# Performance work log

Measured on AMD Instinct MI355X. Metric: run time of the kernel, lower is better.

Reference implementation:

```python
import jax, jax.numpy as jnp
import numpy as np

B, U, SIZE, D_ATT = 8, 1024, 1024, 1024
NEG_INF = -1e38


def setup_inputs() -> dict:
    key = jax.random.key(0)
    ks = jax.random.split(key, 16)
    s = 0.02
    return {
        "x": jax.random.normal(ks[0], (B, U, SIZE), jnp.float32),
        "time_decay": jax.random.normal(ks[1], (D_ATT,), jnp.float32),
        "time_first": jax.random.normal(ks[2], (D_ATT,), jnp.float32),
        "time_mix_key": jax.random.uniform(ks[3], (1, 1, SIZE), jnp.float32),
        "time_mix_value": jax.random.uniform(ks[4], (1, 1, SIZE), jnp.float32),
        "time_mix_receptance": jax.random.uniform(ks[5], (1, 1, SIZE), jnp.float32),
        "W_key": jax.random.normal(ks[6], (SIZE, D_ATT), jnp.float32) * s,
        "b_key": jax.random.normal(ks[7], (D_ATT,), jnp.float32) * s,
        "W_value": jax.random.normal(ks[8], (SIZE, D_ATT), jnp.float32) * s,
        "b_value": jax.random.normal(ks[9], (D_ATT,), jnp.float32) * s,
        "W_receptance": jax.random.normal(ks[10], (SIZE, D_ATT), jnp.float32) * s,
        "b_receptance": jax.random.normal(ks[11], (D_ATT,), jnp.float32) * s,
        "W_output": jax.random.normal(ks[12], (D_ATT, SIZE), jnp.float32) * s,
        "b_output": jax.random.normal(ks[13], (SIZE,), jnp.float32) * s,
    }


def wkv_scan(time_decay, time_first, k, v):
    """Numerically-stable RWKV WKV recurrence. k, v: (B, U, D)."""
    w = -jnp.exp(time_decay)  # (D,)

    def step(carry, kv):
        a, b, p = carry  # each (B, D): numerator, denominator, running max
        kt, vt = kv      # (B, D)
        # output at step t (includes time_first bonus for current token)
        q = jnp.maximum(p, time_first + kt)
        e1 = jnp.exp(p - q)
        e2 = jnp.exp(time_first + kt - q)
        out = (e1 * a + e2 * vt) / (e1 * b + e2)
        # state update (decay by w)
        q2 = jnp.maximum(p + w, kt)
        e1 = jnp.exp(p + w - q2)
        e2 = jnp.exp(kt - q2)
        return (e1 * a + e2 * vt, e1 * b + e2, q2), out

    Bb, Uu, Dd = k.shape
    init = (
        jnp.zeros((Bb, Dd), k.dtype),
        jnp.zeros((Bb, Dd), k.dtype),
        jnp.full((Bb, Dd), NEG_INF, k.dtype),
    )
    _, out = jax.lax.scan(step, init, (k.transpose(1, 0, 2), v.transpose(1, 0, 2)))
    return out.transpose(1, 0, 2)  # (B, U, D)


def reference(x, time_decay, time_first, time_mix_key, time_mix_value,
              time_mix_receptance, W_key, b_key, W_value, b_value,
              W_receptance, b_receptance, W_output, b_output):
    # time_shift: shifted[t] = x[t-1], shifted[0] = 0
    shifted = jnp.pad(x, ((0, 0), (1, 0), (0, 0)))[:, :-1, :]
    k_in = x * time_mix_key + shifted * (1.0 - time_mix_key)
    v_in = x * time_mix_value + shifted * (1.0 - time_mix_value)
    r_in = x * time_mix_receptance + shifted * (1.0 - time_mix_receptance)
    k = jnp.einsum("bus,sd->bud", k_in, W_key) + b_key
    v = jnp.einsum("bus,sd->bud", v_in, W_value) + b_value
    r = jax.nn.sigmoid(jnp.einsum("bus,sd->bud", r_in, W_receptance) + b_receptance)
    wkv = wkv_scan(time_decay, time_first, k, v)
    out = jnp.einsum("bud,ds->bus", r * wkv, W_output) + b_output
    return out
```

## Files before the change

kernel.cpp:

```cpp
#include <hip/hip_runtime.h>
#include <cstdint>
#include <cstddef>

#define B_DIM 8
#define U_DIM 1024
#define SD    1024
#define M_DIM (B_DIM * U_DIM)
#define NC 32
#define CT 32

typedef __attribute__((ext_vector_type(8))) short short8;
typedef __attribute__((ext_vector_type(4))) float f32x4;

typedef __attribute__((address_space(3))) void       lds_t;
typedef const __attribute__((address_space(1))) void glb_t;

__device__ __forceinline__ ushort f2bf(float f) {
    union { float f; uint32_t u; } c; c.f = f;
    uint32_t r = (c.u + 0x7FFFu + ((c.u >> 16) & 1u)) >> 16;
    return (ushort)r;
}
__device__ __forceinline__ float bf2f(ushort h) {
    union { float f; uint32_t u; } c; c.u = ((uint32_t)h) << 16; return c.f;
}

__global__ __launch_bounds__(256)
void wtrans_kernel(const float* __restrict__ Wk, const float* __restrict__ Wv,
                   const float* __restrict__ Wr, const float* __restrict__ Wo,
                   ushort* __restrict__ WT)
{
    __shared__ float t[32][33];
    const float* W = (blockIdx.z == 0) ? Wk : (blockIdx.z == 1) ? Wv
                   : (blockIdx.z == 2) ? Wr : Wo;
    ushort* o = WT + (size_t)blockIdx.z * SD * SD;
    const int tx = threadIdx.x & 31, ty = threadIdx.x >> 5;
    const int k0 = blockIdx.y * 32, n0 = blockIdx.x * 32;
    #pragma unroll
    for (int i = 0; i < 4; ++i)
        t[ty + i * 8][tx] = W[(size_t)(k0 + ty + i * 8) * SD + n0 + tx];
    __syncthreads();
    #pragma unroll
    for (int i = 0; i < 4; ++i)
        o[(size_t)(n0 + ty + i * 8) * SD + k0 + tx] = f2bf(t[tx][ty + i * 8]);
}

__global__ __launch_bounds__(256)
void mix3_kernel(const float* __restrict__ x,
                 const float* __restrict__ mk, const float* __restrict__ mv,
                 const float* __restrict__ mr,
                 ushort* __restrict__ Ak, ushort* __restrict__ Av,
                 ushort* __restrict__ Ar)
{
    const int idx = blockIdx.x * 256 + threadIdx.x;
    const int m = idx >> 8;
    const int s = (idx & 255) << 2;
    const float4 xv = *(const float4*)&x[(size_t)m * SD + s];
    float4 sh = make_float4(0.f, 0.f, 0.f, 0.f);
    if (m & (U_DIM - 1)) sh = *(const float4*)&x[(size_t)(m - 1) * SD + s];
    const float4 dx = make_float4(xv.x - sh.x, xv.y - sh.y, xv.z - sh.z, xv.w - sh.w);
    const size_t off = (size_t)m * SD + s;

    float4 mx;
    ushort4 o;
    mx = *(const float4*)&mk[s];
    o.x = f2bf(sh.x + mx.x * dx.x); o.y = f2bf(sh.y + mx.y * dx.y);
    o.z = f2bf(sh.z + mx.z * dx.z); o.w = f2bf(sh.w + mx.w * dx.w);
    *(ushort4*)&Ak[off] = o;
    mx = *(const float4*)&mv[s];
    o.x = f2bf(sh.x + mx.x * dx.x); o.y = f2bf(sh.y + mx.y * dx.y);
    o.z = f2bf(sh.z + mx.z * dx.z); o.w = f2bf(sh.w + mx.w * dx.w);
    *(ushort4*)&Av[off] = o;
    mx = *(const float4*)&mr[s];
    o.x = f2bf(sh.x + mx.x * dx.x); o.y = f2bf(sh.y + mx.y * dx.y);
    o.z = f2bf(sh.z + mx.z * dx.z); o.w = f2bf(sh.w + mx.w * dx.w);
    *(ushort4*)&Ar[off] = o;
}

__global__ __launch_bounds__(256)
void mix_kernel(const float* __restrict__ x, const float* __restrict__ mix,
                ushort* __restrict__ outA)
{
    const int idx = blockIdx.x * 256 + threadIdx.x;
    const int m = idx >> 8;
    const int s = (idx & 255) << 2;
    const float4 xv = *(const float4*)&x[(size_t)m * SD + s];
    float4 sh = make_float4(0.f, 0.f, 0.f, 0.f);
    if (m & (U_DIM - 1)) sh = *(const float4*)&x[(size_t)(m - 1) * SD + s];
    const float4 mx = *(const float4*)&mix[s];
    ushort4 o;
    o.x = f2bf(sh.x + mx.x * (xv.x - sh.x));
    o.y = f2bf(sh.y + mx.y * (xv.y - sh.y));
    o.z = f2bf(sh.z + mx.z * (xv.z - sh.z));
    o.w = f2bf(sh.w + mx.w * (xv.w - sh.w));
    *(ushort4*)&outA[(size_t)m * SD + s] = o;
}

template<int FUSED>
__global__ __launch_bounds__(256)
void gemm_bf16(const ushort* __restrict__ Abase, const ushort* __restrict__ WT,
               const float* __restrict__ b0, const float* __restrict__ b1,
               const float* __restrict__ b2, void* __restrict__ Cbase)
{
    __shared__ ushort As[2][4096];
    __shared__ ushort Bs[2][4096];

    const int tid = threadIdx.x;
    const int wv = tid >> 6, ln = tid & 63;
    const int m0 = blockIdx.x * 128, n0 = blockIdx.y * 128;
    const int wm = (wv >> 1) * 64, wn = (wv & 1) * 64;

    const ushort* A; const ushort* BT; const float* bias; void* Cout; int dosig;
    if (FUSED == 3) {
        const int z = blockIdx.z;
        A    = Abase + (size_t)z * ((size_t)M_DIM * SD);
        BT   = WT + (size_t)z * ((size_t)SD * SD);
        bias = (z == 0) ? b0 : (z == 1) ? b1 : b2;
        Cout = (void*)((ushort*)Cbase + (size_t)z * ((size_t)M_DIM * SD));
        dosig = (z == 2);
    } else {
        A = Abase; BT = WT; bias = b0; Cout = Cbase; dosig = (FUSED == 1);
    }

    const int srow = tid >> 2;
    const int sq   = tid & 3;
    const int sqs  = sq ^ ((srow >> 1) & 3);
    const size_t gA = (size_t)(m0 + srow) * SD + sqs * 8;
    const size_t gB = (size_t)(n0 + srow) * SD + sqs * 8;
    char* const asb = (char*)As + wv * 1024;
    char* const bsb = (char*)Bs + wv * 1024;

    const int lr  = ln & 15;
    const int lq  = ln >> 4;
    const int sqr = (lr >> 1) & 3;
    const int kof = (lq ^ sqr) * 8;

    f32x4 acc[4][4];
    #pragma unroll
    for (int i = 0; i < 4; ++i)
        #pragma unroll
        for (int j = 0; j < 4; ++j)
            acc[i][j] = (f32x4){0.f, 0.f, 0.f, 0.f};

#define STAGE(buf, k0)                                                              \
    do {                                                                            \
        __builtin_amdgcn_global_load_lds((glb_t*)(A + gA + (k0)),                   \
            (lds_t*)(asb + (buf) * 8192), 16, 0, 0);                                \
        __builtin_amdgcn_global_load_lds((glb_t*)(A + gA + (size_t)64 * SD + (k0)), \
            (lds_t*)(asb + (buf) * 8192 + 4096), 16, 0, 0);                         \
        __builtin_amdgcn_global_load_lds((glb_t*)(BT + gB + (k0)),                  \
            (lds_t*)(bsb + (buf) * 8192), 16, 0, 0);                                \
        __builtin_amdgcn_global_load_lds((glb_t*)(BT + gB + (size_t)64 * SD + (k0)),\
            (lds_t*)(bsb + (buf) * 8192 + 4096), 16, 0, 0);                         \
    } while (0)

#define COMPUTE(buf)                                                                \
    do {                                                                            \
        short8 af[4], bfr[4];                                                       \
        _Pragma("unroll")                                                           \
        for (int mt = 0; mt < 4; ++mt)                                              \
            af[mt] = *(const short8*)&As[buf][(wm + mt * 16 + lr) * 32 + kof];      \
        _Pragma("unroll")                                                           \
        for (int nt = 0; nt < 4; ++nt)                                              \
            bfr[nt] = *(const short8*)&Bs[buf][(wn + nt * 16 + lr) * 32 + kof];     \
        _Pragma("unroll")                                                           \
        for (int mt = 0; mt < 4; ++mt)                                              \
            _Pragma("unroll")                                                       \
            for (int nt = 0; nt < 4; ++nt)                                          \
                acc[mt][nt] = __builtin_amdgcn_mfma_f32_16x16x32_bf16(              \
                    af[mt], bfr[nt], acc[mt][nt], 0, 0, 0);                         \
    } while (0)

    STAGE(0, 0);
    __syncthreads();
    for (int t = 0; t < 30; t += 2) {
        STAGE(1, (size_t)(t + 1) * 32);
        COMPUTE(0);
        __syncthreads();
        STAGE(0, (size_t)(t + 2) * 32);
        COMPUTE(1);
        __syncthreads();
    }
    STAGE(1, (size_t)31 * 32);
    COMPUTE(0);
    __syncthreads();
    COMPUTE(1);

#undef STAGE
#undef COMPUTE

    const int cr = (ln >> 4) * 4;
    const int cc = ln & 15;
    #pragma unroll
    for (int mt = 0; mt < 4; ++mt) {
        #pragma unroll
        for (int nt = 0; nt < 4; ++nt) {
            const int gc = n0 + wn + nt * 16 + cc;
            const float bv = bias[gc];
            #pragma unroll
            for (int j = 0; j < 4; ++j) {
                const int gr = m0 + wm + mt * 16 + cr + j;
                float v = acc[mt][nt][j] + bv;
                if (FUSED == 1 || FUSED == 3) {
                    if (dosig) v = 1.f / (1.f + __expf(-v));
                }
                if (FUSED == 2)
                    ((float*)Cout)[(size_t)gr * SD + gc] = v;
                else
                    ((ushort*)Cout)[(size_t)gr * SD + gc] = f2bf(v);
            }
        }
    }
}

__global__ __launch_bounds__(256)
void scan_local(const ushort* __restrict__ kq, const ushort* __restrict__ vq,
                const float* __restrict__ td,
                float* __restrict__ sa, float* __restrict__ sb, float* __restrict__ sp)
{
    const int idx = blockIdx.x * 256 + threadIdx.x;
    const int ch = idx & (M_DIM - 1);
    const int c  = idx >> 13;
    const int b  = ch >> 10, d = ch & (SD - 1);
    const float w = -__expf(td[d]);
    size_t ptr = (size_t)b * U_DIM * SD + (size_t)(c * CT) * SD + d;

    float a = 0.f, bb = 0.f, p = -1e38f;
    for (int s = 0; s < CT; ++s) {
        const float kt = bf2f(kq[ptr]), vt = bf2f(vq[ptr]);
        const float q2 = fmaxf(p + w, kt);
        const float e1 = __expf(p + w - q2);
        const float e2 = __expf(kt - q2);
        a = e1 * a + e2 * vt; bb = e1 * bb + e2; p = q2;
        ptr += SD;
    }
    sa[idx] = a; sb[idx] = bb; sp[idx] = p;
}

__global__ __launch_bounds__(256)
void scan_prefix(const float* __restrict__ td,
                 float* __restrict__ sa, float* __restrict__ sb, float* __restrict__ sp)
{
    const int ch = blockIdx.x * 256 + threadIdx.x;
    const float wT = -__expf(td[ch & (SD - 1)]) * (float)CT;
    float ca = 0.f, cb = 0.f, cp = -1e38f;
    for (int c = 0; c < NC; ++c) {
        const int i = c * M_DIM + ch;
        const float la = sa[i], lb = sb[i], lp = sp[i];
        sa[i] = ca; sb[i] = cb; sp[i] = cp;
        const float pd = cp + wT;
        const float q  = fmaxf(pd, lp);
        const float e1 = __expf(pd - q);
        const float e2 = __expf(lp - q);
        ca = e1 * ca + e2 * la; cb = e1 * cb + e2 * lb; cp = q;
    }
}

__global__ __launch_bounds__(256)
void scan_out(const ushort* __restrict__ kq, const ushort* __restrict__ vq,
              const ushort* __restrict__ rq,
              const float* __restrict__ td, const float* __restrict__ tfirst,
              const float* __restrict__ sa, const float* __restrict__ sb,
              const float* __restrict__ sp,
              ushort* __restrict__ rw)
{
    const int idx = blockIdx.x * 256 + threadIdx.x;
    const int ch = idx & (M_DIM - 1);
    const int c  = idx >> 13;
    const int b  = ch >> 10, d = ch & (SD - 1);
    const float w  = -__expf(td[d]);
    const float tf = tfirst[d];
    size_t ptr = (size_t)b * U_DIM * SD + (size_t)(c * CT) * SD + d;

    float a = sa[idx], bb = sb[idx], p = sp[idx];
    for (int s = 0; s < CT; ++s) {
        const float kt = bf2f(kq[ptr]), vt = bf2f(vq[ptr]), rt = bf2f(rq[ptr]);
        const float q  = fmaxf(p, tf + kt);
        const float e1 = __expf(p - q);
        const float e2 = __expf(tf + kt - q);
        const float ov = (e1 * a + e2 * vt) * __builtin_amdgcn_rcpf(e1 * bb + e2);
        const float q2  = fmaxf(p + w, kt);
        const float e1b = __expf(p + w - q2);
        const float e2b = __expf(kt - q2);
        a = e1b * a + e2b * vt; bb = e1b * bb + e2b; p = q2;
        rw[ptr] = f2bf(rt * ov);
        ptr += SD;
    }
}

extern "C" void kernel_launch(void* const* d_in, const int* in_sizes, int n_in,
                              void* d_out, int out_size, void* d_ws, size_t ws_size,
                              hipStream_t stream)
{
    (void)in_sizes; (void)n_in; (void)out_size;
    const float* x  = (const float*)d_in[0];
    const float* td = (const float*)d_in[1];
    const float* tf = (const float*)d_in[2];
    const float* mk = (const float*)d_in[3];
    const float* mv = (const float*)d_in[4];
    const float* mr = (const float*)d_in[5];
    const float* Wk = (const float*)d_in[6];
    const float* bk = (const float*)d_in[7];
    const float* Wv = (const float*)d_in[8];
    const float* bv = (const float*)d_in[9];
    const float* Wr = (const float*)d_in[10];
    const float* br = (const float*)d_in[11];
    const float* Wo = (const float*)d_in[12];
    const float* bo = (const float*)d_in[13];
    float* out = (float*)d_out;

    const size_t NE = (size_t)M_DIM * SD;
    char* ws = (char*)d_ws;

    const dim3 gg1(M_DIM / 128, SD / 128, 1);
    const dim3 gg3(M_DIM / 128, SD / 128, 3);

    if (ws_size >= ((size_t)108 << 20)) {
        ushort* WT  = (ushort*)ws;
        ushort* Ak  = (ushort*)(ws + ((size_t)8   << 20));
        ushort* kvr = (ushort*)(ws + ((size_t)56  << 20));
        float*  sa  = (float*)(ws + ((size_t)104 << 20));
        float*  sb  = (float*)(ws + ((size_t)105 << 20));
        float*  sp  = (float*)(ws + ((size_t)106 << 20));
        ushort* kbuf = kvr;
        ushort* vbuf = kvr + NE;
        ushort* rbuf = kvr + 2 * NE;
        ushort* rwkv = Ak;

        wtrans_kernel<<<dim3(32, 32, 4), 256, 0, stream>>>(Wk, Wv, Wr, Wo, WT);
        mix3_kernel<<<8192, 256, 0, stream>>>(x, mk, mv, mr, Ak, Ak + NE, Ak + 2 * NE);
        gemm_bf16<3><<<gg3, 256, 0, stream>>>(Ak, WT, bk, bv, br, kvr);

        scan_local <<<(M_DIM * NC) / 256, 256, 0, stream>>>(kbuf, vbuf, td, sa, sb, sp);
        scan_prefix<<<M_DIM / 256, 256, 0, stream>>>(td, sa, sb, sp);
        scan_out   <<<(M_DIM * NC) / 256, 256, 0, stream>>>(kbuf, vbuf, rbuf, td, tf,
                                                            sa, sb, sp, rwkv);

        gemm_bf16<2><<<gg1, 256, 0, stream>>>(rwkv, WT + 3 * NE / 8, bo, bo, bo, out);
    } else {
        ushort* WT   = (ushort*)ws;
        ushort* Abuf = (ushort*)(ws + ((size_t)8  << 20));
        ushort* kbuf = (ushort*)(ws + ((size_t)24 << 20));
        ushort* vbuf = (ushort*)(ws + ((size_t)40 << 20));
        ushort* rbuf = (ushort*)(ws + ((size_t)56 << 20));
        float*  sa   = (float*)(ws + ((size_t)72 << 20));
        float*  sb   = (float*)(ws + ((size_t)73 << 20));
        float*  sp   = (float*)(ws + ((size_t)74 << 20));
        ushort* rwkv = Abuf;
        const size_t WS = (size_t)SD * SD;

        wtrans_kernel<<<dim3(32, 32, 4), 256, 0, stream>>>(Wk, Wv, Wr, Wo, WT);
        mix_kernel<<<8192, 256, 0, stream>>>(x, mk, Abuf);
        gemm_bf16<0><<<gg1, 256, 0, stream>>>(Abuf, WT, bk, bk, bk, kbuf);
        mix_kernel<<<8192, 256, 0, stream>>>(x, mv, Abuf);
        gemm_bf16<0><<<gg1, 256, 0, stream>>>(Abuf, WT + WS, bv, bv, bv, vbuf);
        mix_kernel<<<8192, 256, 0, stream>>>(x, mr, Abuf);
        gemm_bf16<1><<<gg1, 256, 0, stream>>>(Abuf, WT + 2 * WS, br, br, br, rbuf);

        scan_local <<<(M_DIM * NC) / 256, 256, 0, stream>>>(kbuf, vbuf, td, sa, sb, sp);
        scan_prefix<<<M_DIM / 256, 256, 0, stream>>>(td, sa, sb, sp);
        scan_out   <<<(M_DIM * NC) / 256, 256, 0, stream>>>(kbuf, vbuf, rbuf, td, tf,
                                                            sa, sb, sp, rwkv);

        gemm_bf16<2><<<gg1, 256, 0, stream>>>(rwkv, WT + 3 * WS, bo, bo, bo, out);
    }
}
```

Before: 169.9 us.

## Replace 128x128 GEMM with 256x256 tile, 512-thread, phased-pipeline bf16 GEMM

The bf16 MFMA GEMM moves from 128x128 tiles with 4 waves to 256x256 tiles with 8 waves and K-step 64. Staging is split into quadrant phases that interleave global-to-LDS loads with MFMA work, using explicit barriers, vmcnt waits and setprio. Block IDs are remapped so that consecutive blocks land on the same XCD. The larger tiles are meant to raise operand reuse and cut global traffic. In exchange they need much more LDS (128KB) and accumulator registers, which limits occupancy.

```diff
diff --git a/kernel.cpp b/kernel.cpp
--- a/kernel.cpp
+++ b/kernel.cpp
@@ -96,118 +96,160 @@
 }
 
 template<int FUSED>
-__global__ __launch_bounds__(256)
-void gemm_bf16(const ushort* __restrict__ Abase, const ushort* __restrict__ WT,
-               const float* __restrict__ b0, const float* __restrict__ b1,
-               const float* __restrict__ b2, void* __restrict__ Cbase)
-{
-    __shared__ ushort As[2][4096];
-    __shared__ ushort Bs[2][4096];
+__global__ __launch_bounds__(512)
+void gemm256(const ushort* __restrict__ Abase, const ushort* __restrict__ WTbase,
+             const float* __restrict__ b0, const float* __restrict__ b1,
+             const float* __restrict__ b2, void* __restrict__ Cbase)
+{
+    __shared__ ushort LA[2][2][2][128][32];
+    __shared__ ushort LB[2][2][2][128][32];
 
     const int tid = threadIdx.x;
-    const int wv = tid >> 6, ln = tid & 63;
-    const int m0 = blockIdx.x * 128, n0 = blockIdx.y * 128;
-    const int wm = (wv >> 1) * 64, wn = (wv & 1) * 64;
+    const int wv  = tid >> 6, ln = tid & 63;
+
+    const int nwg = (int)(gridDim.x * gridDim.y * gridDim.z);
+    int bid = (int)blockIdx.x + 32 * ((int)blockIdx.y + 4 * (int)blockIdx.z);
+    const int cpx = nwg >> 3;
+    const int s_  = (bid & 7) * cpx + (bid >> 3);
+    const int mb  = s_ & 31;
+    const int nbz = s_ >> 5;
+    const int nb  = nbz & 3;
+    const int z   = nbz >> 2;
+    const int m0 = mb * 256, n0 = nb * 256;
 
     const ushort* A; const ushort* BT; const float* bias; void* Cout; int dosig;
     if (FUSED == 3) {
-        const int z = blockIdx.z;
         A    = Abase + (size_t)z * ((size_t)M_DIM * SD);
-        BT   = WT + (size_t)z * ((size_t)SD * SD);
+        BT   = WTbase + (size_t)z * ((size_t)SD * SD);
         bias = (z == 0) ? b0 : (z == 1) ? b1 : b2;
         Cout = (void*)((ushort*)Cbase + (size_t)z * ((size_t)M_DIM * SD));
         dosig = (z == 2);
     } else {
-        A = Abase; BT = WT; bias = b0; Cout = Cbase; dosig = (FUSED == 1);
+        A = Abase; BT = WTbase; bias = b0; Cout = Cbase; dosig = (FUSED == 1);
     }
 
     const int srow = tid >> 2;
-    const int sq   = tid & 3;
-    const int sqs  = sq ^ ((srow >> 1) & 3);
-    const size_t gA = (size_t)(m0 + srow) * SD + sqs * 8;
-    const size_t gB = (size_t)(n0 + srow) * SD + sqs * 8;
-    char* const asb = (char*)As + wv * 1024;
-    char* const bsb = (char*)Bs + wv * 1024;
-
+    const int ssw  = (((tid & 3) ^ ((tid >> 3) & 3)) << 3);
+    const size_t aS0 = (size_t)(m0 + srow) * SD + ssw;
+    const size_t aS1 = (size_t)(m0 + 128 + srow) * SD + ssw;
+    const size_t bS0 = (size_t)(n0 + srow) * SD + ssw;
+    const size_t bS1 = (size_t)(n0 + 128 + srow) * SD + ssw;
+    char* const laW = (char*)LA + wv * 1024;
+    char* const lbW = (char*)LB + wv * 1024;
+
+    const char* LAc = (const char*)LA;
+    const char* LBc = (const char*)LB;
     const int lr  = ln & 15;
-    const int lq  = ln >> 4;
-    const int sqr = (lr >> 1) & 3;
-    const int kof = (lq ^ sqr) * 8;
-
-    f32x4 acc[4][4];
-    #pragma unroll
-    for (int i = 0; i < 4; ++i)
+    const int kof = (((ln >> 4) ^ ((lr >> 1) & 3)) << 4);
+    const int aRd = ((wv >> 2) << 12) + lr * 64 + kof;
+    const int bRd = ((wv & 3) << 11) + lr * 64 + kof;
+
+    f32x4 acc[8][4];
+    #pragma unroll
+    for (int i = 0; i < 8; ++i)
         #pragma unroll
         for (int j = 0; j < 4; ++j)
             acc[i][j] = (f32x4){0.f, 0.f, 0.f, 0.f};
 
-#define STAGE(buf, k0)                                                              \
+#define STG_A(buf, half, kt)                                                        \
+    do { const size_t s0 = ((half) ? aS1 : aS0) + (size_t)(kt) * 64;                \
+        __builtin_amdgcn_global_load_lds((glb_t*)(A + s0),                          \
+            (lds_t*)(laW + (buf) * 32768 + (half) * 16384), 16, 0, 0);              \
+        __builtin_amdgcn_global_load_lds((glb_t*)(A + s0 + 32),                     \
+            (lds_t*)(laW + (buf) * 32768 + (half) * 16384 + 8192), 16, 0, 0);       \
+    } while (0)
+
+#define STG_B(buf, half, kt)                                                        \
+    do { const size_t s0 = ((half) ? bS1 : bS0) + (size_t)(kt) * 64;                \
+        __builtin_amdgcn_global_load_lds((glb_t*)(BT + s0),                         \
+            (lds_t*)(lbW + (buf) * 32768 + (half) * 16384), 16, 0, 0);              \
+        __builtin_amdgcn_global_load_lds((glb_t*)(BT + s0 + 32),                    \
+            (lds_t*)(lbW + (buf) * 32768 + (half) * 16384 + 8192), 16, 0, 0);       \
+    } while (0)
+
+#define PHASE(buf, qm, qn, STG, DOVM)                                               \
     do {                                                                            \
-        __builtin_amdgcn_global_load_lds((glb_t*)(A + gA + (k0)),                   \
-            (lds_t*)(asb + (buf) * 8192), 16, 0, 0);                                \
-        __builtin_amdgcn_global_load_lds((glb_t*)(A + gA + (size_t)64 * SD + (k0)), \
-            (lds_t*)(asb + (buf) * 8192 + 4096), 16, 0, 0);                         \
-        __builtin_amdgcn_global_load_lds((glb_t*)(BT + gB + (k0)),                  \
-            (lds_t*)(bsb + (buf) * 8192), 16, 0, 0);                                \
-        __builtin_amdgcn_global_load_lds((glb_t*)(BT + gB + (size_t)64 * SD + (k0)),\
-            (lds_t*)(bsb + (buf) * 8192 + 4096), 16, 0, 0);                         \
-    } while (0)
-
-#define COMPUTE(buf)                                                                \
-    do {                                                                            \
-        short8 af[4], bfr[4];                                                       \
+        short8 af[4][2], bq[2][2];                                                  \
         _Pragma("unroll")                                                           \
-        for (int mt = 0; mt < 4; ++mt)                                              \
-            af[mt] = *(const short8*)&As[buf][(wm + mt * 16 + lr) * 32 + kof];      \
+        for (int mt = 0; mt < 4; ++mt) {                                            \
+            af[mt][0] = *(const short8*)(LAc + (buf) * 32768 + (qm) * 16384         \
+                                         + mt * 1024 + aRd);                        \
+            af[mt][1] = *(const short8*)(LAc + (buf) * 32768 + (qm) * 16384         \
+                                         + 8192 + mt * 1024 + aRd);                 \
+        }                                                                           \
         _Pragma("unroll")                                                           \
-        for (int nt = 0; nt < 4; ++nt)                                              \
-            bfr[nt] = *(const short8*)&Bs[buf][(wn + nt * 16 + lr) * 32 + kof];     \
+        for (int nt = 0; nt < 2; ++nt) {                                            \
+            bq[nt][0] = *(const short8*)(LBc + (buf) * 32768 + (qn) * 16384         \
+                                         + nt * 1024 + bRd);                        \
+            bq[nt][1] = *(const short8*)(LBc + (buf) * 32768 + (qn) * 16384         \
+                                         + 8192 + nt * 1024 + bRd);                 \
+        }                                                                           \
+        STG;                                                                        \
+        __builtin_amdgcn_s_barrier();                                               \
+        __builtin_amdgcn_s_setprio(1);                                              \
         _Pragma("unroll")                                                           \
         for (int mt = 0; mt < 4; ++mt)                                              \
             _Pragma("unroll")                                                       \
-            for (int nt = 0; nt < 4; ++nt)                                          \
-                acc[mt][nt] = __builtin_amdgcn_mfma_f32_16x16x32_bf16(              \
-                    af[mt], bfr[nt], acc[mt][nt], 0, 0, 0);                         \
+            for (int nt = 0; nt < 2; ++nt) {                                        \
+                acc[(qm) * 4 + mt][(qn) * 2 + nt] =                                 \
+                    __builtin_amdgcn_mfma_f32_16x16x32_bf16(af[mt][0], bq[nt][0],   \
+                        acc[(qm) * 4 + mt][(qn) * 2 + nt], 0, 0, 0);                \
+                acc[(qm) * 4 + mt][(qn) * 2 + nt] =                                 \
+                    __builtin_amdgcn_mfma_f32_16x16x32_bf16(af[mt][1], bq[nt][1],   \
+                        acc[(qm) * 4 + mt][(qn) * 2 + nt], 0, 0, 0);                \
+            }                                                                       \
+        __builtin_amdgcn_s_setprio(0);                                              \
+        if (DOVM) { asm volatile("s_waitcnt vmcnt(4)" ::: "memory"); }              \
+        __builtin_amdgcn_s_barrier();                                               \
     } while (0)
 
-    STAGE(0, 0);
-    __syncthreads();
-    for (int t = 0; t < 30; t += 2) {
-        STAGE(1, (size_t)(t + 1) * 32);
-        COMPUTE(0);
-        __syncthreads();
-        STAGE(0, (size_t)(t + 2) * 32);
-        COMPUTE(1);
-        __syncthreads();
-    }
-    STAGE(1, (size_t)31 * 32);
-    COMPUTE(0);
-    __syncthreads();
-    COMPUTE(1);
-
-#undef STAGE
-#undef COMPUTE
+    STG_A(0, 0, 0); STG_B(0, 0, 0);
+    STG_A(0, 1, 0); STG_B(0, 1, 0);
+    STG_A(1, 0, 1); STG_B(1, 0, 1);
+    asm volatile("s_waitcnt vmcnt(4)" ::: "memory");
+    __builtin_amdgcn_s_barrier();
+
+    for (int i = 0; i < 8; ++i) {
+        const int t  = 2 * i;
+        const int t2 = (t + 2 < 16) ? t + 2 : 15;
+        const int t3 = (t + 3 < 16) ? t + 3 : 15;
+        PHASE(0, 0, 0, STG_A(1, 1, t + 1), 0);
+        PHASE(0, 0, 1, STG_B(1, 1, t + 1), 0);
+        PHASE(0, 1, 0, STG_A(0, 0, t2), 0);
+        PHASE(0, 1, 1, STG_B(0, 0, t2), 1);
+        PHASE(1, 0, 0, STG_A(0, 1, t2), 0);
+        PHASE(1, 0, 1, STG_B(0, 1, t2), 0);
+        PHASE(1, 1, 0, STG_A(1, 0, t3), 0);
+        PHASE(1, 1, 1, STG_B(1, 0, t3), 1);
+    }
+
+#undef PHASE
+#undef STG_A
+#undef STG_B
 
     const int cr = (ln >> 4) * 4;
     const int cc = ln & 15;
-    #pragma unroll
-    for (int mt = 0; mt < 4; ++mt) {
+    const int wm = (wv >> 2) * 64;
+    const int wn = (wv & 3) * 32;
+    #pragma unroll
+    for (int qm = 0; qm < 2; ++qm)
+    #pragma unroll
+    for (int qn = 0; qn < 2; ++qn)
+    #pragma unroll
+    for (int mt = 0; mt < 4; ++mt)
+    #pragma unroll
+    for (int nt = 0; nt < 2; ++nt) {
+        const int gc = n0 + qn * 128 + wn + nt * 16 + cc;
+        const float bv = bias[gc];
         #pragma unroll
-        for (int nt = 0; nt < 4; ++nt) {
-            const int gc = n0 + wn + nt * 16 + cc;
-            const float bv = bias[gc];
-            #pragma unroll
-            for (int j = 0; j < 4; ++j) {
-                const int gr = m0 + wm + mt * 16 + cr + j;
-                float v = acc[mt][nt][j] + bv;
-                if (FUSED == 1 || FUSED == 3) {
-                    if (dosig) v = 1.f / (1.f + __expf(-v));
-                }
-                if (FUSED == 2)
-                    ((float*)Cout)[(size_t)gr * SD + gc] = v;
-                else
-                    ((ushort*)Cout)[(size_t)gr * SD + gc] = f2bf(v);
-            }
+        for (int j = 0; j < 4; ++j) {
+            const int gr = m0 + qm * 128 + wm + mt * 16 + cr + j;
+            float v = acc[qm * 4 + mt][qn * 2 + nt][j] + bv;
+            if (FUSED == 1 || FUSED == 3) { if (dosig) v = 1.f / (1.f + __expf(-v)); }
+            if (FUSED == 2)
+                ((float*)Cout)[(size_t)gr * SD + gc] = v;
+            else
+                ((ushort*)Cout)[(size_t)gr * SD + gc] = f2bf(v);
         }
     }
 }
@@ -309,10 +351,11 @@
     float* out = (float*)d_out;
 
     const size_t NE = (size_t)M_DIM * SD;
+    const size_t WS = (size_t)SD * SD;
     char* ws = (char*)d_ws;
 
-    const dim3 gg1(M_DIM / 128, SD / 128, 1);
-    const dim3 gg3(M_DIM / 128, SD / 128, 3);
+    const dim3 gg1(32, 4, 1);
+    const dim3 gg3(32, 4, 3);
 
     if (ws_size >= ((size_t)108 << 20)) {
         ushort* WT  = (ushort*)ws;
@@ -328,14 +371,14 @@
 
         wtrans_kernel<<<dim3(32, 32, 4), 256, 0, stream>>>(Wk, Wv, Wr, Wo, WT);
         mix3_kernel<<<8192, 256, 0, stream>>>(x, mk, mv, mr, Ak, Ak + NE, Ak + 2 * NE);
-        gemm_bf16<3><<<gg3, 256, 0, stream>>>(Ak, WT, bk, bv, br, kvr);
+        gemm256<3><<<gg3, 512, 0, stream>>>(Ak, WT, bk, bv, br, kvr);
 
         scan_local <<<(M_DIM * NC) / 256, 256, 0, stream>>>(kbuf, vbuf, td, sa, sb, sp);
         scan_prefix<<<M_DIM / 256, 256, 0, stream>>>(td, sa, sb, sp);
         scan_out   <<<(M_DIM * NC) / 256, 256, 0, stream>>>(kbuf, vbuf, rbuf, td, tf,
                                                             sa, sb, sp, rwkv);
 
-        gemm_bf16<2><<<gg1, 256, 0, stream>>>(rwkv, WT + 3 * NE / 8, bo, bo, bo, out);
+        gemm256<2><<<gg1, 512, 0, stream>>>(rwkv, WT + 3 * WS, bo, bo, bo, out);
     } else {
         ushort* WT   = (ushort*)ws;
         ushort* Abuf = (ushort*)(ws + ((size_t)8  << 20));
@@ -346,21 +389,20 @@
         float*  sb   = (float*)(ws + ((size_t)73 << 20));
         float*  sp   = (float*)(ws + ((size_t)74 << 20));
         ushort* rwkv = Abuf;
-        const size_t WS = (size_t)SD * SD;
 
         wtrans_kernel<<<dim3(32, 32, 4), 256, 0, stream>>>(Wk, Wv, Wr, Wo, WT);
         mix_kernel<<<8192, 256, 0, stream>>>(x, mk, Abuf);
-        gemm_bf16<0><<<gg1, 256, 0, stream>>>(Abuf, WT, bk, bk, bk, kbuf);
+        gemm256<0><<<gg1, 512, 0, stream>>>(Abuf, WT, bk, bk, bk, kbuf);
         mix_kernel<<<8192, 256, 0, stream>>>(x, mv, Abuf);
-        gemm_bf16<0><<<gg1, 256, 0, stream>>>(Abuf, WT + WS, bv, bv, bv, vbuf);
+        gemm256<0><<<gg1, 512, 0, stream>>>(Abuf, WT + WS, bv, bv, bv, vbuf);
         mix_kernel<<<8192, 256, 0, stream>>>(x, mr, Abuf);
-        gemm_bf16<1><<<gg1, 256, 0, stream>>>(Abuf, WT + 2 * WS, br, br, br, rbuf);
+        gemm256<1><<<gg1, 512, 0, stream>>>(Abuf, WT + 2 * WS, br, br, br, rbuf);
 
         scan_local <<<(M_DIM * NC) / 256, 256, 0, stream>>>(kbuf, vbuf, td, sa, sb, sp);
         scan_prefix<<<M_DIM / 256, 256, 0, stream>>>(td, sa, sb, sp);
         scan_out   <<<(M_DIM * NC) / 256, 256, 0, stream>>>(kbuf, vbuf, rbuf, td, tf,
                                                             sa, sb, sp, rwkv);
 
-        gemm_bf16<2><<<gg1, 256, 0, stream>>>(rwkv, WT + 3 * WS, bo, bo, bo, out);
-    }
-}
+        gemm256<2><<<gg1, 512, 0, stream>>>(rwkv, WT + 3 * WS, bo, bo, bo, out);
+    }
+}
```

New measurement: 185.5 us. 9.2% more time.

## Rewrite bf16 GEMM with 256x128 tiles, triple-buffered LDS and XCD-aware block swizzle

Applied to the files above, without the earlier changes.

Replaces the 128x128 double-buffered GEMM with a 512-thread kernel computing 256x128 tiles over a 64-wide K step, split into two 32-wide phases. Global-to-LDS loads are triple-buffered and prefetched two steps ahead, with explicit vmcnt waits and raw barriers instead of __syncthreads. MFMA sections run under raised s_setprio. Block IDs are remapped round-robin across the 8 XCDs so neighbouring tiles share L2. It aims to improve operand reuse and hide load latency, at the cost of about 144KB of LDS per block (one block per CU) and fragile manual waitcnt accounting.

```diff
diff --git a/kernel.cpp b/kernel.cpp
--- a/kernel.cpp
+++ b/kernel.cpp
@@ -96,43 +96,53 @@
 }
 
 template<int FUSED>
-__global__ __launch_bounds__(256)
-void gemm_bf16(const ushort* __restrict__ Abase, const ushort* __restrict__ WT,
-               const float* __restrict__ b0, const float* __restrict__ b1,
-               const float* __restrict__ b2, void* __restrict__ Cbase)
-{
-    __shared__ ushort As[2][4096];
-    __shared__ ushort Bs[2][4096];
+__global__ __launch_bounds__(512)
+void gemm_big(const ushort* __restrict__ Abase, const ushort* __restrict__ WTbase,
+              const float* __restrict__ b0, const float* __restrict__ b1,
+              const float* __restrict__ b2, void* __restrict__ Cbase)
+{
+    __shared__ ushort LA[3][2][256][32];
+    __shared__ ushort LB[3][2][128][32];
 
     const int tid = threadIdx.x;
     const int wv = tid >> 6, ln = tid & 63;
-    const int m0 = blockIdx.x * 128, n0 = blockIdx.y * 128;
-    const int wm = (wv >> 1) * 64, wn = (wv & 1) * 64;
+    const int wr = wv >> 1, wc = wv & 1;
+
+    const int nwg = (int)(gridDim.x * gridDim.y * gridDim.z);
+    const int bid = (int)blockIdx.x +
+                    (int)gridDim.x * ((int)blockIdx.y + (int)gridDim.y * (int)blockIdx.z);
+    const int s_  = (bid & 7) * (nwg >> 3) + (bid >> 3);
+    const int mb  = s_ & 31;
+    const int nb  = (s_ >> 5) & 7;
+    const int z   = s_ >> 8;
+    const int m0 = mb * 256, n0 = nb * 128;
 
     const ushort* A; const ushort* BT; const float* bias; void* Cout; int dosig;
     if (FUSED == 3) {
-        const int z = blockIdx.z;
         A    = Abase + (size_t)z * ((size_t)M_DIM * SD);
-        BT   = WT + (size_t)z * ((size_t)SD * SD);
+        BT   = WTbase + (size_t)z * ((size_t)SD * SD);
         bias = (z == 0) ? b0 : (z == 1) ? b1 : b2;
         Cout = (void*)((ushort*)Cbase + (size_t)z * ((size_t)M_DIM * SD));
         dosig = (z == 2);
     } else {
-        A = Abase; BT = WT; bias = b0; Cout = Cbase; dosig = (FUSED == 1);
+        A = Abase; BT = WTbase; bias = b0; Cout = Cbase; dosig = (FUSED == 1);
     }
 
     const int srow = tid >> 2;
-    const int sq   = tid & 3;
-    const int sqs  = sq ^ ((srow >> 1) & 3);
-    const size_t gA = (size_t)(m0 + srow) * SD + sqs * 8;
-    const size_t gB = (size_t)(n0 + srow) * SD + sqs * 8;
-    char* const asb = (char*)As + wv * 1024;
-    char* const bsb = (char*)Bs + wv * 1024;
-
+    const int ssw  = ((tid & 3) ^ ((srow >> 1) & 3)) << 3;
+    const ushort* aSrc0 = A  + (size_t)(m0 + srow) * SD + ssw;
+    const ushort* aSrc1 = aSrc0 + (size_t)128 * SD;
+    const ushort* bSrc  = BT + (size_t)(n0 + srow) * SD + ssw;
+    char* const laW = (char*)LA + wv * 1024;
+    char* const lbW = (char*)LB + wv * 1024;
+
+    const char* LAc = (const char*)LA;
+    const char* LBc = (const char*)LB;
     const int lr  = ln & 15;
     const int lq  = ln >> 4;
-    const int sqr = (lr >> 1) & 3;
-    const int kof = (lq ^ sqr) * 8;
+    const int kof = ((lq ^ ((lr >> 1) & 3)) << 4);
+    const int aRd = wr * 4096 + lr * 64 + kof;
+    const int bRd = wc * 4096 + lr * 64 + kof;
 
     f32x4 acc[4][4];
     #pragma unroll
@@ -141,73 +151,74 @@
         for (int j = 0; j < 4; ++j)
             acc[i][j] = (f32x4){0.f, 0.f, 0.f, 0.f};
 
-#define STAGE(buf, k0)                                                              \
+#define STG(bufS, ks, kt)                                                           \
+    do { const int off = (kt) * 64 + (ks) * 32;                                     \
+        __builtin_amdgcn_global_load_lds((glb_t*)(aSrc0 + off),                     \
+            (lds_t*)(laW + (bufS) * 32768 + (ks) * 16384), 16, 0, 0);               \
+        __builtin_amdgcn_global_load_lds((glb_t*)(aSrc1 + off),                     \
+            (lds_t*)(laW + (bufS) * 32768 + (ks) * 16384 + 8192), 16, 0, 0);        \
+        __builtin_amdgcn_global_load_lds((glb_t*)(bSrc + off),                      \
+            (lds_t*)(lbW + (bufS) * 16384 + (ks) * 8192), 16, 0, 0);                \
+    } while (0)
+
+#define PHASE(bR, ks, bS, kt)                                                       \
     do {                                                                            \
-        __builtin_amdgcn_global_load_lds((glb_t*)(A + gA + (k0)),                   \
-            (lds_t*)(asb + (buf) * 8192), 16, 0, 0);                                \
-        __builtin_amdgcn_global_load_lds((glb_t*)(A + gA + (size_t)64 * SD + (k0)), \
-            (lds_t*)(asb + (buf) * 8192 + 4096), 16, 0, 0);                         \
-        __builtin_amdgcn_global_load_lds((glb_t*)(BT + gB + (k0)),                  \
-            (lds_t*)(bsb + (buf) * 8192), 16, 0, 0);                                \
-        __builtin_amdgcn_global_load_lds((glb_t*)(BT + gB + (size_t)64 * SD + (k0)),\
-            (lds_t*)(bsb + (buf) * 8192 + 4096), 16, 0, 0);                         \
-    } while (0)
-
-#define COMPUTE(buf)                                                                \
-    do {                                                                            \
-        short8 af[4], bfr[4];                                                       \
+        short8 af[4], bq[4];                                                        \
         _Pragma("unroll")                                                           \
         for (int mt = 0; mt < 4; ++mt)                                              \
-            af[mt] = *(const short8*)&As[buf][(wm + mt * 16 + lr) * 32 + kof];      \
+            af[mt] = *(const short8*)(LAc + (bR) * 32768 + (ks) * 16384             \
+                                      + mt * 1024 + aRd);                           \
         _Pragma("unroll")                                                           \
         for (int nt = 0; nt < 4; ++nt)                                              \
-            bfr[nt] = *(const short8*)&Bs[buf][(wn + nt * 16 + lr) * 32 + kof];     \
+            bq[nt] = *(const short8*)(LBc + (bR) * 16384 + (ks) * 8192              \
+                                      + nt * 1024 + bRd);                           \
+        STG(bS, ks, kt);                                                            \
+        __builtin_amdgcn_s_barrier();                                               \
+        __builtin_amdgcn_s_setprio(1);                                              \
         _Pragma("unroll")                                                           \
         for (int mt = 0; mt < 4; ++mt)                                              \
             _Pragma("unroll")                                                       \
             for (int nt = 0; nt < 4; ++nt)                                          \
                 acc[mt][nt] = __builtin_amdgcn_mfma_f32_16x16x32_bf16(              \
-                    af[mt], bfr[nt], acc[mt][nt], 0, 0, 0);                         \
+                    af[mt], bq[nt], acc[mt][nt], 0, 0, 0);                          \
+        __builtin_amdgcn_s_setprio(0);                                              \
+        asm volatile("s_waitcnt vmcnt(9)" ::: "memory");                            \
+        __builtin_amdgcn_s_barrier();                                               \
     } while (0)
 
-    STAGE(0, 0);
-    __syncthreads();
-    for (int t = 0; t < 30; t += 2) {
-        STAGE(1, (size_t)(t + 1) * 32);
-        COMPUTE(0);
-        __syncthreads();
-        STAGE(0, (size_t)(t + 2) * 32);
-        COMPUTE(1);
-        __syncthreads();
-    }
-    STAGE(1, (size_t)31 * 32);
-    COMPUTE(0);
-    __syncthreads();
-    COMPUTE(1);
-
-#undef STAGE
-#undef COMPUTE
-
-    const int cr = (ln >> 4) * 4;
-    const int cc = ln & 15;
-    #pragma unroll
-    for (int mt = 0; mt < 4; ++mt) {
+    STG(0, 0, 0); STG(0, 1, 0);
+    STG(1, 0, 1); STG(1, 1, 1);
+    asm volatile("s_waitcnt vmcnt(9)" ::: "memory");
+    __builtin_amdgcn_s_barrier();
+
+    for (int t = 0; t < 16; ++t) {
+        const int bR = t % 3;
+        const int tn = (t + 2 < 16) ? t + 2 : 15;
+        const int bS = (t + 2) % 3;
+        PHASE(bR, 0, bS, tn);
+        PHASE(bR, 1, bS, tn);
+    }
+
+#undef PHASE
+#undef STG
+
+    const int cr = lq * 4;
+    const int cc = lr;
+    #pragma unroll
+    for (int mt = 0; mt < 4; ++mt)
+    #pragma unroll
+    for (int nt = 0; nt < 4; ++nt) {
+        const int gc = n0 + wc * 64 + nt * 16 + cc;
+        const float bv = bias[gc];
         #pragma unroll
-        for (int nt = 0; nt < 4; ++nt) {
-            const int gc = n0 + wn + nt * 16 + cc;
-            const float bv = bias[gc];
-            #pragma unroll
-            for (int j = 0; j < 4; ++j) {
-                const int gr = m0 + wm + mt * 16 + cr + j;
-                float v = acc[mt][nt][j] + bv;
-                if (FUSED == 1 || FUSED == 3) {
-                    if (dosig) v = 1.f / (1.f + __expf(-v));
-                }
-                if (FUSED == 2)
-                    ((float*)Cout)[(size_t)gr * SD + gc] = v;
-                else
-                    ((ushort*)Cout)[(size_t)gr * SD + gc] = f2bf(v);
-            }
+        for (int j = 0; j < 4; ++j) {
+            const int gr = m0 + wr * 64 + mt * 16 + cr + j;
+            float v = acc[mt][nt][j] + bv;
+            if (FUSED == 1 || FUSED == 3) { if (dosig) v = 1.f / (1.f + __expf(-v)); }
+            if (FUSED == 2)
+                ((float*)Cout)[(size_t)gr * SD + gc] = v;
+            else
+                ((ushort*)Cout)[(size_t)gr * SD + gc] = f2bf(v);
         }
     }
 }
@@ -309,10 +320,11 @@
     float* out = (float*)d_out;
 
     const size_t NE = (size_t)M_DIM * SD;
+    const size_t WS = (size_t)SD * SD;
     char* ws = (char*)d_ws;
 
-    const dim3 gg1(M_DIM / 128, SD / 128, 1);
-    const dim3 gg3(M_DIM / 128, SD / 128, 3);
+    const dim3 gg1(32, 8, 1);
+    const dim3 gg3(32, 8, 3);
 
     if (ws_size >= ((size_t)108 << 20)) {
         ushort* WT  = (ushort*)ws;
@@ -328,14 +340,14 @@
 
         wtrans_kernel<<<dim3(32, 32, 4), 256, 0, stream>>>(Wk, Wv, Wr, Wo, WT);
         mix3_kernel<<<8192, 256, 0, stream>>>(x, mk, mv, mr, Ak, Ak + NE, Ak + 2 * NE);
-        gemm_bf16<3><<<gg3, 256, 0, stream>>>(Ak, WT, bk, bv, br, kvr);
+        gemm_big<3><<<gg3, 512, 0, stream>>>(Ak, WT, bk, bv, br, kvr);
 
         scan_local <<<(M_DIM * NC) / 256, 256, 0, stream>>>(kbuf, vbuf, td, sa, sb, sp);
         scan_prefix<<<M_DIM / 256, 256, 0, stream>>>(td, sa, sb, sp);
         scan_out   <<<(M_DIM * NC) / 256, 256, 0, stream>>>(kbuf, vbuf, rbuf, td, tf,
                                                             sa, sb, sp, rwkv);
 
-        gemm_bf16<2><<<gg1, 256, 0, stream>>>(rwkv, WT + 3 * NE / 8, bo, bo, bo, out);
+        gemm_big<2><<<gg1, 512, 0, stream>>>(rwkv, WT + 3 * WS, bo, bo, bo, out);
     } else {
         ushort* WT   = (ushort*)ws;
         ushort* Abuf = (ushort*)(ws + ((size_t)8  << 20));
@@ -346,21 +358,20 @@
         float*  sb   = (float*)(ws + ((size_t)73 << 20));
         float*  sp   = (float*)(ws + ((size_t)74 << 20));
         ushort* rwkv = Abuf;
-        const size_t WS = (size_t)SD * SD;
 
         wtrans_kernel<<<dim3(32, 32, 4), 256, 0, stream>>>(Wk, Wv, Wr, Wo, WT);
         mix_kernel<<<8192, 256, 0, stream>>>(x, mk, Abuf);
-        gemm_bf16<0><<<gg1, 256, 0, stream>>>(Abuf, WT, bk, bk, bk, kbuf);
+        gemm_big<0><<<gg1, 512, 0, stream>>>(Abuf, WT, bk, bk, bk, kbuf);
         mix_kernel<<<8192, 256, 0, stream>>>(x, mv, Abuf);
-        gemm_bf16<0><<<gg1, 256, 0, stream>>>(Abuf, WT + WS, bv, bv, bv, vbuf);
+        gemm_big<0><<<gg1, 512, 0, stream>>>(Abuf, WT + WS, bv, bv, bv, vbuf);
         mix_kernel<<<8192, 256, 0, stream>>>(x, mr, Abuf);
-        gemm_bf16<1><<<gg1, 256, 0, stream>>>(Abuf, WT + 2 * WS, br, br, br, rbuf);
+        gemm_big<1><<<gg1, 512, 0, stream>>>(Abuf, WT + 2 * WS, br, br, br, rbuf);
 
         scan_local <<<(M_DIM * NC) / 256, 256, 0, stream>>>(kbuf, vbuf, td, sa, sb, sp);
         scan_prefix<<<M_DIM / 256, 256, 0, stream>>>(td, sa, sb, sp);
         scan_out   <<<(M_DIM * NC) / 256, 256, 0, stream>>>(kbuf, vbuf, rbuf, td, tf,
                                                             sa, sb, sp, rwkv);
 
-        gemm_bf16<2><<<gg1, 256, 0, stream>>>(rwkv, WT + 3 * WS, bo, bo, bo, out);
-    }
-}
+        gemm_big<2><<<gg1, 512, 0, stream>>>(rwkv, WT + 3 * WS, bo, bo, bo, out);
+    }
+}
```

New measurement: 176.9 us. 1.04x slower.
